# Kernel tuning notes

Measured on AMD Instinct MI355X. Metric: run time of the kernel, lower is better.

## Reference

```python
import jax, jax.numpy as jnp
import numpy as np

N_NODES = 50000
N_EDGES = 500000
D_FEAT = 128


def setup_inputs() -> dict:
    key = jax.random.key(0)
    k1, k2 = jax.random.split(key)
    x = jax.random.normal(k1, (N_NODES, D_FEAT), dtype=jnp.float32)
    edge_index = jax.random.randint(k2, (2, N_EDGES), 0, N_NODES, dtype=jnp.int64)
    return {"x": x, "edge_index": edge_index}


def reference(x, edge_index):
    # flow='source_to_target': row = edge_index[0] (source j), col = edge_index[1] (target i)
    row, col = edge_index[0], edge_index[1]
    # message(x_j) = x_j ; aggregate = scatter-add at target indices ; update = identity
    messages = jnp.take(x, row, axis=0)            # [E, D] gather
    out = jax.ops.segment_sum(messages, col, num_segments=x.shape[0])  # [N, D]
    return out
```

## Files before the change

kernel.cpp:

```cpp
#include <hip/hip_runtime.h>
#include <hip/hip_bf16.h>


#define D_FEAT 128
#define MAXDEG 32

typedef unsigned short u16;
typedef unsigned int u32;

__device__ __forceinline__ u16 f2bf(float f) {
    union { __hip_bfloat16 h; u16 u; } c;
    c.h = __float2bfloat16(f);
    return c.u;
}
__device__ __forceinline__ float bflo(u32 u) { return __uint_as_float(u << 16); }
__device__ __forceinline__ float bfhi(u32 u) { return __uint_as_float(u & 0xffff0000u); }

__device__ __forceinline__ void addrow(float acc[8], const uint4& v) {
    acc[0] += bflo(v.x); acc[1] += bfhi(v.x);
    acc[2] += bflo(v.y); acc[3] += bfhi(v.y);
    acc[4] += bflo(v.z); acc[5] += bfhi(v.z);
    acc[6] += bflo(v.w); acc[7] += bfhi(v.w);
}

__global__ __launch_bounds__(256) void fused_kernel(const float* __restrict__ x,
                                                    u16* __restrict__ xb, int nf4,
                                                    const int* __restrict__ row,
                                                    const int* __restrict__ col,
                                                    int* __restrict__ cnt,
                                                    u16* __restrict__ srclist,
                                                    int* __restrict__ ovf,
                                                    int* __restrict__ ovfcnt,
                                                    int E, int ovfcap,
                                                    int fill_blocks, int aligned) {
    if ((int)blockIdx.x < fill_blocks) {
        const int t = blockIdx.x * 256 + threadIdx.x;
        const int e0 = t * 4;
        if (e0 >= E) return;
        int d[4], s[4], p[4], ne;
        if (aligned && e0 + 4 <= E) {
            const int4 dv = *reinterpret_cast<const int4*>(col + e0);
            const int4 sv = *reinterpret_cast<const int4*>(row + e0);
            d[0] = dv.x; d[1] = dv.y; d[2] = dv.z; d[3] = dv.w;
            s[0] = sv.x; s[1] = sv.y; s[2] = sv.z; s[3] = sv.w;
            ne = 4;
        } else {
            ne = E - e0; if (ne > 4) ne = 4;
            for (int k = 0; k < ne; ++k) { d[k] = col[e0 + k]; s[k] = row[e0 + k]; }
        }
        #pragma unroll
        for (int k = 0; k < 4; ++k)
            if (k < ne) p[k] = atomicAdd(&cnt[d[k]], 1);
        #pragma unroll
        for (int k = 0; k < 4; ++k) {
            if (k < ne) {
                if (p[k] < MAXDEG) {
                    srclist[(size_t)d[k] * MAXDEG + p[k]] = (u16)s[k];
                } else {
                    int o = atomicAdd(ovfcnt, 1);
                    if (o < ovfcap) { ovf[2 * o] = d[k]; ovf[2 * o + 1] = s[k]; }
                }
            }
        }
    } else {
        const int i = ((int)blockIdx.x - fill_blocks) * 256 + threadIdx.x;
        if (i < nf4) {
            const float4 v = reinterpret_cast<const float4*>(x)[i];
            ushort4 o;
            o.x = f2bf(v.x); o.y = f2bf(v.y); o.z = f2bf(v.z); o.w = f2bf(v.w);
            reinterpret_cast<ushort4*>(xb)[i] = o;
        }
    }
}

__global__ __launch_bounds__(256) void gatherq_kernel(const u16* __restrict__ xb,
                                                      const int* __restrict__ cnt,
                                                      const u16* __restrict__ srclist,
                                                      const int* __restrict__ ovf,
                                                      const int* __restrict__ ovfcnt,
                                                      float* __restrict__ out,
                                                      int N, int ovfcap) {
    const int wid  = (blockIdx.x * blockDim.x + threadIdx.x) >> 6;
    const int lane = threadIdx.x & 63;
    if (wid >= N) return;
    const int q = lane >> 4;
    const int c = lane & 15;
    const int rawdeg = cnt[wid];
    const int deg = rawdeg > MAXDEG ? MAXDEG : rawdeg;
    const u16* bucket = srclist + (size_t)wid * MAXDEG;
    const int bval = (int)bucket[lane & 31];

    float acc[8] = {0.f, 0.f, 0.f, 0.f, 0.f, 0.f, 0.f, 0.f};

    int j = 0;
    for (; j + 8 <= deg; j += 8) {
        const int i0 = __shfl(bval, j + q, 64);
        const int i1 = __shfl(bval, j + 4 + q, 64);
        const uint4 w0 = *reinterpret_cast<const uint4*>(xb + (size_t)i0 * D_FEAT + c * 8);
        const uint4 w1 = *reinterpret_cast<const uint4*>(xb + (size_t)i1 * D_FEAT + c * 8);
        addrow(acc, w0);
        addrow(acc, w1);
    }
    if (j + 4 <= deg) {
        const int i0 = __shfl(bval, j + q, 64);
        const uint4 w0 = *reinterpret_cast<const uint4*>(xb + (size_t)i0 * D_FEAT + c * 8);
        addrow(acc, w0);
        j += 4;
    }
    {
        const int r = deg - j;
        const int i0 = __shfl(bval, j + q, 64);
        if (q < r) {
            const uint4 w0 = *reinterpret_cast<const uint4*>(xb + (size_t)i0 * D_FEAT + c * 8);
            addrow(acc, w0);
        }
    }

    if (rawdeg > MAXDEG) {
        int novf = *ovfcnt;
        if (novf > ovfcap) novf = ovfcap;
        for (int k = 0; k < novf; ++k) {
            if (ovf[2 * k] == wid && q == 0) {
                const int s = ovf[2 * k + 1];
                const uint4 w = *reinterpret_cast<const uint4*>(xb + (size_t)s * D_FEAT + c * 8);
                addrow(acc, w);
            }
        }
    }

    #pragma unroll
    for (int k = 0; k < 8; ++k) {
        acc[k] += __shfl_xor(acc[k], 16, 64);
        acc[k] += __shfl_xor(acc[k], 32, 64);
    }
    if (q == 0) {
        float* o = out + (size_t)wid * D_FEAT + c * 8;
        *reinterpret_cast<float4*>(o)     = make_float4(acc[0], acc[1], acc[2], acc[3]);
        *reinterpret_cast<float4*>(o + 4) = make_float4(acc[4], acc[5], acc[6], acc[7]);
    }
}

__global__ void mp_scatter_kernel(const float* __restrict__ x,
                                  const int* __restrict__ row,
                                  const int* __restrict__ col,
                                  float* __restrict__ out, int n_edges) {
    const int t = blockIdx.x * blockDim.x + threadIdx.x;
    const int e = t >> 5;
    const int c = t & 31;
    if (e >= n_edges) return;
    const float4 v = *reinterpret_cast<const float4*>(
        x + (size_t)row[e] * D_FEAT + (size_t)c * 4);
    float* o = out + (size_t)col[e] * D_FEAT + (size_t)c * 4;
    atomicAdd(o + 0, v.x);
    atomicAdd(o + 1, v.y);
    atomicAdd(o + 2, v.z);
    atomicAdd(o + 3, v.w);
}

extern "C" void kernel_launch(void* const* d_in, const int* in_sizes, int n_in,
                              void* d_out, int out_size, void* d_ws, size_t ws_size,
                              hipStream_t stream) {
    const float* x   = (const float*)d_in[0];
    const int*   ei  = (const int*)d_in[1];
    float*       out = (float*)d_out;

    const int E = in_sizes[1] / 2;
    const int N = out_size / D_FEAT;
    const int* row = ei;
    const int* col = ei + E;

    const size_t cnt_bytes = ((size_t)N + 1) * 4;
    const size_t xb_off    = (cnt_bytes + 255) & ~(size_t)255;
    const size_t xb_bytes  = (size_t)N * D_FEAT * 2;
    const size_t src_off   = (xb_off + xb_bytes + 255) & ~(size_t)255;
    const size_t src_bytes = (size_t)N * MAXDEG * 2;
    const size_t ovf_off   = (src_off + src_bytes + 255) & ~(size_t)255;
    const size_t needed    = ovf_off + 2ull * (size_t)E * 4;

    if (ws_size < needed || N > 65535) {
        (void)hipMemsetAsync(d_out, 0, (size_t)out_size * sizeof(float), stream);
        const int total = E * 32;
        mp_scatter_kernel<<<(total + 255) / 256, 256, 0, stream>>>(x, row, col, out, E);
        return;
    }

    char* wsb     = (char*)d_ws;
    int*  cnt     = (int*)wsb;
    int*  ovfcnt  = cnt + N;
    u16*  xb      = (u16*)(wsb + xb_off);
    u16*  srclist = (u16*)(wsb + src_off);
    int*  ovf     = (int*)(wsb + ovf_off);

    (void)hipMemsetAsync(cnt, 0, cnt_bytes, stream);

    const int fill_threads = (E + 3) / 4;
    const int fill_blocks  = (fill_threads + 255) / 256;
    const int nf4          = N * D_FEAT / 4;
    const int conv_blocks  = (nf4 + 255) / 256;
    const int aligned      = ((E & 3) == 0) ? 1 : 0;
    fused_kernel<<<fill_blocks + conv_blocks, 256, 0, stream>>>(
        x, xb, nf4, row, col, cnt, srclist, ovf, ovfcnt, E, E, fill_blocks, aligned);

    const int total = N * 64;
    gatherq_kernel<<<(total + 255) / 256, 256, 0, stream>>>(xb, cnt, srclist,
                                                            ovf, ovfcnt, out, N, E);
}
```

Before: 125.9 us.

## Split gather feature columns into XCD-affine slices for per-die L2 reuse

```diff
diff --git a/kernel.cpp b/kernel.cpp
--- a/kernel.cpp
+++ b/kernel.cpp
@@ -15,13 +15,6 @@
 }
 __device__ __forceinline__ float bflo(u32 u) { return __uint_as_float(u << 16); }
 __device__ __forceinline__ float bfhi(u32 u) { return __uint_as_float(u & 0xffff0000u); }
-
-__device__ __forceinline__ void addrow(float acc[8], const uint4& v) {
-    acc[0] += bflo(v.x); acc[1] += bfhi(v.x);
-    acc[2] += bflo(v.y); acc[3] += bfhi(v.y);
-    acc[4] += bflo(v.z); acc[5] += bfhi(v.z);
-    acc[6] += bflo(v.w); acc[7] += bfhi(v.w);
-}
 
 __global__ __launch_bounds__(256) void fused_kernel(const float* __restrict__ x,
                                                     u16* __restrict__ xb, int nf4,
@@ -73,46 +66,53 @@
     }
 }
 
-__global__ __launch_bounds__(256) void gatherq_kernel(const u16* __restrict__ xb,
+__global__ __launch_bounds__(256) void gathers_kernel(const u16* __restrict__ xb,
                                                       const int* __restrict__ cnt,
                                                       const u16* __restrict__ srclist,
                                                       const int* __restrict__ ovf,
                                                       const int* __restrict__ ovfcnt,
                                                       float* __restrict__ out,
                                                       int N, int ovfcap) {
-    const int wid  = (blockIdx.x * blockDim.x + threadIdx.x) >> 6;
+    const int bid   = blockIdx.x;
+    const int xcd   = bid & 7;
+    const int slice = xcd >> 1;
+    const int group = ((bid >> 3) << 1) | (bid & 1);
+    const int wav   = threadIdx.x >> 6;
+    const int wid   = group * 4 + wav;
+    if (wid >= N) return;
     const int lane = threadIdx.x & 63;
-    if (wid >= N) return;
-    const int q = lane >> 4;
-    const int c = lane & 15;
+    const int q  = lane >> 4;
+    const int c2 = lane & 15;
+
     const int rawdeg = cnt[wid];
     const int deg = rawdeg > MAXDEG ? MAXDEG : rawdeg;
     const u16* bucket = srclist + (size_t)wid * MAXDEG;
     const int bval = (int)bucket[lane & 31];
 
-    float acc[8] = {0.f, 0.f, 0.f, 0.f, 0.f, 0.f, 0.f, 0.f};
+    const size_t colbase = (size_t)slice * 32 + (size_t)c2 * 2;
+    float a0 = 0.f, a1 = 0.f;
 
     int j = 0;
     for (; j + 8 <= deg; j += 8) {
         const int i0 = __shfl(bval, j + q, 64);
         const int i1 = __shfl(bval, j + 4 + q, 64);
-        const uint4 w0 = *reinterpret_cast<const uint4*>(xb + (size_t)i0 * D_FEAT + c * 8);
-        const uint4 w1 = *reinterpret_cast<const uint4*>(xb + (size_t)i1 * D_FEAT + c * 8);
-        addrow(acc, w0);
-        addrow(acc, w1);
+        const u32 w0 = *reinterpret_cast<const u32*>(xb + (size_t)i0 * D_FEAT + colbase);
+        const u32 w1 = *reinterpret_cast<const u32*>(xb + (size_t)i1 * D_FEAT + colbase);
+        a0 += bflo(w0) + bflo(w1);
+        a1 += bfhi(w0) + bfhi(w1);
     }
     if (j + 4 <= deg) {
         const int i0 = __shfl(bval, j + q, 64);
-        const uint4 w0 = *reinterpret_cast<const uint4*>(xb + (size_t)i0 * D_FEAT + c * 8);
-        addrow(acc, w0);
+        const u32 w0 = *reinterpret_cast<const u32*>(xb + (size_t)i0 * D_FEAT + colbase);
+        a0 += bflo(w0); a1 += bfhi(w0);
         j += 4;
     }
     {
         const int r = deg - j;
         const int i0 = __shfl(bval, j + q, 64);
         if (q < r) {
-            const uint4 w0 = *reinterpret_cast<const uint4*>(xb + (size_t)i0 * D_FEAT + c * 8);
-            addrow(acc, w0);
+            const u32 w0 = *reinterpret_cast<const u32*>(xb + (size_t)i0 * D_FEAT + colbase);
+            a0 += bflo(w0); a1 += bfhi(w0);
         }
     }
 
@@ -122,21 +122,19 @@
         for (int k = 0; k < novf; ++k) {
             if (ovf[2 * k] == wid && q == 0) {
                 const int s = ovf[2 * k + 1];
-                const uint4 w = *reinterpret_cast<const uint4*>(xb + (size_t)s * D_FEAT + c * 8);
-                addrow(acc, w);
+                const u32 w = *reinterpret_cast<const u32*>(xb + (size_t)s * D_FEAT + colbase);
+                a0 += bflo(w); a1 += bfhi(w);
             }
         }
     }
 
-    #pragma unroll
-    for (int k = 0; k < 8; ++k) {
-        acc[k] += __shfl_xor(acc[k], 16, 64);
-        acc[k] += __shfl_xor(acc[k], 32, 64);
-    }
+    a0 += __shfl_xor(a0, 16, 64);
+    a1 += __shfl_xor(a1, 16, 64);
+    a0 += __shfl_xor(a0, 32, 64);
+    a1 += __shfl_xor(a1, 32, 64);
     if (q == 0) {
-        float* o = out + (size_t)wid * D_FEAT + c * 8;
-        *reinterpret_cast<float4*>(o)     = make_float4(acc[0], acc[1], acc[2], acc[3]);
-        *reinterpret_cast<float4*>(o + 4) = make_float4(acc[4], acc[5], acc[6], acc[7]);
+        float* o = out + (size_t)wid * D_FEAT + slice * 32 + c2 * 2;
+        *reinterpret_cast<float2*>(o) = make_float2(a0, a1);
     }
 }
 
@@ -201,7 +199,8 @@
     fused_kernel<<<fill_blocks + conv_blocks, 256, 0, stream>>>(
         x, xb, nf4, row, col, cnt, srclist, ovf, ovfcnt, E, E, fill_blocks, aligned);
 
-    const int total = N * 64;
-    gatherq_kernel<<<(total + 255) / 256, 256, 0, stream>>>(xb, cnt, srclist,
-                                                            ovf, ovfcnt, out, N, E);
-}
+    const int blocks_per_slice = (N + 3) / 4;
+    const int half             = (blocks_per_slice + 1) / 2;
+    const int grid             = 8 * half;
+    gathers_kernel<<<grid, 256, 0, stream>>>(xb, cnt, srclist, ovf, ovfcnt, out, N, E);
+}
```

Result: slower. 151.4 us (+20.2%).
